# Kernel optimization log

Hardware: AMD Instinct MI355X
Metric: run time of the kernel (lower is better)

## Reference

```python
import jax, jax.numpy as jnp
import numpy as np

D_MODEL = 1024
NUM_HEADS = 16
D_K = D_MODEL // NUM_HEADS


def setup_inputs() -> dict:
    key = jax.random.key(0)
    ks = jax.random.split(key, 9)
    B, S = 2, 2048
    s = 1.0 / np.sqrt(D_MODEL)
    inp = {
        "x": jax.random.normal(ks[0], (B, S, D_MODEL), dtype=jnp.float32),
        "Wq": jax.random.normal(ks[1], (D_MODEL, D_MODEL), dtype=jnp.float32) * s,
        "bq": jnp.zeros((D_MODEL,), dtype=jnp.float32),
        "Wk": jax.random.normal(ks[2], (D_MODEL, D_MODEL), dtype=jnp.float32) * s,
        "bk": jnp.zeros((D_MODEL,), dtype=jnp.float32),
        "Wv": jax.random.normal(ks[3], (D_MODEL, D_MODEL), dtype=jnp.float32) * s,
        "bv": jnp.zeros((D_MODEL,), dtype=jnp.float32),
        "Wo": jax.random.normal(ks[4], (D_MODEL, D_MODEL), dtype=jnp.float32) * s,
        "bo": jnpp if False else jnp.zeros((D_MODEL,), dtype=jnp.float32),
    }
    return inp


def reference(x, Wq, bq, Wk, bk, Wv, bv, Wo, bo):
    B, S, _ = x.shape
    H, Dk = NUM_HEADS, D_K

    def proj(W, b):
        # [B,S,D] -> [B,H,S,Dk]
        return (x @ W + b).reshape(B, S, H, Dk).transpose(0, 2, 1, 3)

    Q = proj(Wq, bq)
    K = proj(Wk, bk)
    V = proj(Wv, bv)

    scores = jnp.einsum("bhqd,bhkd->bhqk", Q, K) / np.sqrt(Dk)
    attn = jax.nn.softmax(scores, axis=-1)  # no mask, dropout p=0 (eval)
    out = jnp.einsum("bhqk,bhkd->bhqd", attn, V)
    out = out.transpose(0, 2, 1, 3).reshape(B, S, D_MODEL)
    return out @ Wo + bo
```

## Files before the change

### kernel.cpp

```cpp
#include <hip/hip_runtime.h>
#include <hip/hip_bf16.h>
#include <cstdint>
#include <math.h>

#define D_MODEL 1024
#define NHEADS  16
#define DK      64
#define BATCH   2
#define SEQ     2048
#define M_TOTAL (BATCH*SEQ)
#define NSPLIT  2
#define NTS     (SEQ/64/NSPLIT)

using f32x4  = __attribute__((ext_vector_type(4)))  float;
using f32x16 = __attribute__((ext_vector_type(16))) float;
using s16x8  = __attribute__((ext_vector_type(8)))  short;

#define CSC (0.125f * 1.44269504088896341f)

__device__ __forceinline__ unsigned short bf16r(float f) {
    __hip_bfloat16 h = __float2bfloat16(f);
    return *(unsigned short*)&h;
}
__device__ __forceinline__ uint32_t cvtpk(float lo, float hi) {
    uint32_t r;
    asm("v_cvt_pk_bf16_f32 %0, %1, %2" : "=v"(r) : "v"(lo), "v"(hi));
    return r;
}
__device__ __forceinline__ float b2f(unsigned short u) {
    uint32_t x = (uint32_t)u << 16;
    float f;
    __builtin_memcpy(&f, &x, 4);
    return f;
}

__global__ __launch_bounds__(256) void conv_all(const float* __restrict__ x,
                                                unsigned short* __restrict__ xb,
                                                const float* __restrict__ W0, const float* __restrict__ W1,
                                                const float* __restrict__ W2, const float* __restrict__ W3,
                                                unsigned short* __restrict__ T0, unsigned short* __restrict__ T1,
                                                unsigned short* __restrict__ T2, unsigned short* __restrict__ T3)
{
    __shared__ float tile[32][33];
    const int bid = blockIdx.x;
    const int t   = threadIdx.x;

    if (bid < 2048) {
        const size_t i = ((size_t)bid * 256 + t) * 8;
        const float4 a = *(const float4*)(x + i);
        const float4 b = *(const float4*)(x + i + 4);
        ushort4 r0, r1;
        r0.x = bf16r(a.x); r0.y = bf16r(a.y); r0.z = bf16r(a.z); r0.w = bf16r(a.w);
        r1.x = bf16r(b.x); r1.y = bf16r(b.y); r1.z = bf16r(b.z); r1.w = bf16r(b.w);
        *(ushort4*)(xb + i)     = r0;
        *(ushort4*)(xb + i + 4) = r1;
        return;
    }

    const int b2   = bid - 2048;
    const int z    = b2 >> 10;
    const int rest = b2 & 1023;
    const int kblk = rest & 31;
    const int nblk = rest >> 5;
    const float* W; unsigned short* T;
    switch (z) {
        case 0: W = W0; T = T0; break;
        case 1: W = W1; T = T1; break;
        case 2: W = W2; T = T2; break;
        default: W = W3; T = T3; break;
    }
    const int r  = t >> 3;
    const int c4 = (t & 7) * 4;
    const int k0 = kblk * 32;
    const int n0 = nblk * 32;

    const float4 v = *(const float4*)(W + (size_t)(k0 + r) * 1024 + n0 + c4);
    tile[r][c4 + 0] = v.x; tile[r][c4 + 1] = v.y; tile[r][c4 + 2] = v.z; tile[r][c4 + 3] = v.w;
    __syncthreads();
    ushort4 o;
    o.x = bf16r(tile[c4 + 0][r]);
    o.y = bf16r(tile[c4 + 1][r]);
    o.z = bf16r(tile[c4 + 2][r]);
    o.w = bf16r(tile[c4 + 3][r]);
    *(ushort4*)(T + (size_t)(n0 + r) * 1024 + k0 + c4) = o;
}

template<int OUT_BF16>
__device__ __forceinline__ void gemm_mfma_body(const unsigned short* __restrict__ A,
                                               const unsigned short* __restrict__ Bt,
                                               const float* __restrict__ bias,
                                               void* __restrict__ C,
                                               float oscale, int m0, int n0)
{
    __shared__ unsigned short As[128 * 64];
    __shared__ unsigned short Bs[128 * 64];

    const int t    = threadIdx.x;
    const int w    = t >> 6;
    const int lane = t & 63;
    const int ln   = lane & 15;
    const int g    = lane >> 4;
    const int wr   = w >> 1, wc = w & 1;

    f32x4 acc[4][4];
#pragma unroll
    for (int mi = 0; mi < 4; ++mi)
#pragma unroll
        for (int ni = 0; ni < 4; ++ni)
#pragma unroll
            for (int j = 0; j < 4; ++j) acc[mi][ni][j] = 0.f;

    const int lrow = lane >> 3;
    const int lchk = (lane & 7) ^ lrow;
    const unsigned short* Ag = A  + (size_t)(m0 + w * 32 + lrow) * 1024 + lchk * 8;
    const unsigned short* Bg = Bt + (size_t)(n0 + w * 32 + lrow) * 1024 + lchk * 8;

    for (int kt = 0; kt < 16; ++kt) {
        const int k0 = kt * 64;
#pragma unroll
        for (int i = 0; i < 4; ++i) {
            __builtin_amdgcn_global_load_lds(Ag + (size_t)i * 8 * 1024 + k0,
                                             &As[(w * 32 + i * 8) * 64], 16, 0, 0);
            __builtin_amdgcn_global_load_lds(Bg + (size_t)i * 8 * 1024 + k0,
                                             &Bs[(w * 32 + i * 8) * 64], 16, 0, 0);
        }
        __syncthreads();

#pragma unroll
        for (int ks = 0; ks < 2; ++ks) {
            s16x8 af[4], bf[4];
#pragma unroll
            for (int mi = 0; mi < 4; ++mi) {
                const int row = wr * 64 + mi * 16 + ln;
                af[mi] = *(const s16x8*)((const char*)As + row * 128 +
                                         (((ks * 4 + g) ^ (ln & 7)) * 16));
            }
#pragma unroll
            for (int ni = 0; ni < 4; ++ni) {
                const int row = wc * 64 + ni * 16 + ln;
                bf[ni] = *(const s16x8*)((const char*)Bs + row * 128 +
                                         (((ks * 4 + g) ^ (ln & 7)) * 16));
            }
#pragma unroll
            for (int mi = 0; mi < 4; ++mi)
#pragma unroll
                for (int ni = 0; ni < 4; ++ni)
                    acc[mi][ni] = __builtin_amdgcn_mfma_f32_16x16x32_bf16(
                        af[mi], bf[ni], acc[mi][ni], 0, 0, 0);
        }
        __syncthreads();
    }

#pragma unroll
    for (int ni = 0; ni < 4; ++ni) {
        const int n = n0 + wc * 64 + ni * 16 + ln;
        const float bn = bias[n];
#pragma unroll
        for (int mi = 0; mi < 4; ++mi) {
            const int m = m0 + wr * 64 + mi * 16 + g * 4;
#pragma unroll
            for (int j = 0; j < 4; ++j) {
                const float v = (acc[mi][ni][j] + bn) * oscale;
                if constexpr (OUT_BF16)
                    ((unsigned short*)C)[(size_t)(m + j) * 1024 + n] = bf16r(v);
                else
                    ((float*)C)[(size_t)(m + j) * 1024 + n] = v;
            }
        }
    }
}

__global__ __launch_bounds__(256) void qkv_mfma(const unsigned short* __restrict__ xb,
                                                const unsigned short* __restrict__ Wqt, const float* __restrict__ bq,
                                                const unsigned short* __restrict__ Wkt, const float* __restrict__ bk,
                                                const unsigned short* __restrict__ Wvt, const float* __restrict__ bv,
                                                unsigned short* __restrict__ Q,
                                                unsigned short* __restrict__ K,
                                                unsigned short* __restrict__ V)
{
    const int bid = blockIdx.x;
    const int m   = bid / 24;
    const int rr  = bid - m * 24;
    const int z   = rr >> 3;
    const int n   = rr & 7;
    const int m0  = m * 128;
    const int n0  = n * 128;

    if (z == 0)      gemm_mfma_body<1>(xb, Wqt, bq, Q, CSC, m0, n0);
    else if (z == 1) gemm_mfma_body<1>(xb, Wkt, bk, K, 1.0f, m0, n0);
    else             gemm_mfma_body<1>(xb, Wvt, bv, V, 1.0f, m0, n0);
}

__global__ __launch_bounds__(256) void oproj_mfma(const unsigned short* __restrict__ Ab,
                                                  const unsigned short* __restrict__ Wot,
                                                  const float* __restrict__ bo,
                                                  float* __restrict__ C)
{
    gemm_mfma_body<0>(Ab, Wot, bo, C, 1.0f, blockIdx.y * 128, blockIdx.x * 128);
}

__global__ __launch_bounds__(256, 4) void attn_mfma(const unsigned short* __restrict__ Qb,
                                                    const unsigned short* __restrict__ Kb,
                                                    const unsigned short* __restrict__ Vb,
                                                    unsigned short* __restrict__ O0,
                                                    unsigned short* __restrict__ O1,
                                                    float* __restrict__ lbuf)
{
    __shared__ unsigned short Klds [64 * 64];
    __shared__ unsigned short Vtlds[64 * 64];

    const int t   = threadIdx.x;
    const int wid = t >> 6;
    const int l   = t & 63;
    const int q32 = l & 31;
    const int hi  = l >> 5;

    const int bid = blockIdx.x;
    const int grp = bid & 63;
    const int qb  = bid >> 6;
    const int bh  = grp >> 1;
    const int sp  = grp & 1;
    const int b   = bh >> 4;
    const int h   = bh & 15;
    const int qbase = qb * 128 + wid * 32;
    const size_t qrow = (size_t)(b * SEQ + qbase + q32);
    const size_t kv0  = (size_t)(b * SEQ) + (size_t)sp * (SEQ / NSPLIT);

    s16x8 qf[4];
    {
        const unsigned short* qp = Qb + qrow * D_MODEL + h * DK + 8 * hi;
#pragma unroll
        for (int ks = 0; ks < 4; ++ks) qf[ks] = *(const s16x8*)(qp + 16 * ks);
    }

    f32x16 ot0, ot1;
#pragma unroll
    for (int i = 0; i < 16; ++i) { ot0[i] = 0.f; ot1[i] = 0.f; }
    float lsum = 0.f;

    const int skey = t >> 3;
    const int sc8  = t & 7;
    const int vk2  = 2 * (t & 31);
    const int pk2  = (vk2 & ~12) | ((vk2 & 4) << 1) | ((vk2 & 8) >> 1);
    const int vd0  = 8 * (t >> 5);
    const unsigned short* Kg = Kb + (kv0 + skey) * D_MODEL + h * DK + 8 * sc8;
    const unsigned short* Vg = Vb + (kv0 + vk2) * D_MODEL + h * DK + vd0;
    char* const kw0 = (char*)Klds + skey * 128        + 16 * (sc8 ^ (skey & 7));
    char* const kw1 = (char*)Klds + (skey + 32) * 128 + 16 * (sc8 ^ (skey & 7));

    s16x8 kr0, kr1, vr0, vr1;

    auto load_regs = [&](int kt) {
        const size_t off = (size_t)kt * 64 * D_MODEL;
        kr0 = *(const s16x8*)(Kg + off);
        kr1 = *(const s16x8*)(Kg + off + (size_t)32 * D_MODEL);
        vr0 = *(const s16x8*)(Vg + off);
        vr1 = *(const s16x8*)(Vg + off + D_MODEL);
    };
    auto write_stage = [&]() {
        *(s16x8*)kw0 = kr0;
        *(s16x8*)kw1 = kr1;
#pragma unroll
        for (int i = 0; i < 8; ++i) {
            const int d = vd0 + i;
            const uint32_t val = (uint32_t)(unsigned short)vr0[i] |
                                 ((uint32_t)(unsigned short)vr1[i] << 16);
            *(uint32_t*)((char*)Vtlds + d * 128 +
                         16 * ((pk2 >> 3) ^ (d & 7)) + (pk2 & 7) * 2) = val;
        }
    };

    load_regs(0);
    write_stage();
    __syncthreads();

    for (int kt = 0; kt < NTS; ++kt) {
        if (kt < NTS - 1) load_regs(kt + 1);

        f32x16 s0, s1;
#pragma unroll
        for (int i = 0; i < 16; ++i) { s0[i] = 0.f; s1[i] = 0.f; }
        __builtin_amdgcn_s_setprio(1);
#pragma unroll
        for (int ks = 0; ks < 4; ++ks) {
            const int c = hi + 2 * ks;
            const s16x8 a0 = *(const s16x8*)((char*)Klds + q32 * 128 + 16 * (c ^ (q32 & 7)));
            const s16x8 a1 = *(const s16x8*)((char*)Klds + (q32 + 32) * 128 + 16 * (c ^ (q32 & 7)));
            s0 = __builtin_amdgcn_mfma_f32_32x32x16_bf16(a0, qf[ks], s0, 0, 0, 0);
            s1 = __builtin_amdgcn_mfma_f32_32x32x16_bf16(a1, qf[ks], s1, 0, 0, 0);
        }
        __builtin_amdgcn_s_setprio(0);

        float la = 0.f, lb = 0.f, lc = 0.f, ld = 0.f;
#pragma unroll
        for (int i = 0; i < 4; ++i) {
            s0[4 * i + 0] = exp2f(s0[4 * i + 0]); la += s0[4 * i + 0];
            s0[4 * i + 1] = exp2f(s0[4 * i + 1]); lb += s0[4 * i + 1];
            s0[4 * i + 2] = exp2f(s0[4 * i + 2]); lc += s0[4 * i + 2];
            s0[4 * i + 3] = exp2f(s0[4 * i + 3]); ld += s0[4 * i + 3];
            s1[4 * i + 0] = exp2f(s1[4 * i + 0]); la += s1[4 * i + 0];
            s1[4 * i + 1] = exp2f(s1[4 * i + 1]); lb += s1[4 * i + 1];
            s1[4 * i + 2] = exp2f(s1[4 * i + 2]); lc += s1[4 * i + 2];
            s1[4 * i + 3] = exp2f(s1[4 * i + 3]); ld += s1[4 * i + 3];
        }
        lsum += (la + lb) + (lc + ld);

        s16x8 pf[4];
        {
            union { uint32_t u[4]; s16x8 v; } F;
#pragma unroll
            for (int e = 0; e < 4; ++e) F.u[e] = cvtpk(s0[2 * e], s0[2 * e + 1]);
            pf[0] = F.v;
#pragma unroll
            for (int e = 0; e < 4; ++e) F.u[e] = cvtpk(s0[8 + 2 * e], s0[9 + 2 * e]);
            pf[1] = F.v;
#pragma unroll
            for (int e = 0; e < 4; ++e) F.u[e] = cvtpk(s1[2 * e], s1[2 * e + 1]);
            pf[2] = F.v;
#pragma unroll
            for (int e = 0; e < 4; ++e) F.u[e] = cvtpk(s1[8 + 2 * e], s1[9 + 2 * e]);
            pf[3] = F.v;
        }

        __builtin_amdgcn_s_setprio(1);
#pragma unroll
        for (int ks = 0; ks < 4; ++ks) {
            const int c = hi + 2 * ks;
            const s16x8 av0 = *(const s16x8*)((char*)Vtlds + q32 * 128 + 16 * (c ^ (q32 & 7)));
            const s16x8 av1 = *(const s16x8*)((char*)Vtlds + (q32 + 32) * 128 + 16 * (c ^ (q32 & 7)));
            ot0 = __builtin_amdgcn_mfma_f32_32x32x16_bf16(av0, pf[ks], ot0, 0, 0, 0);
            ot1 = __builtin_amdgcn_mfma_f32_32x32x16_bf16(av1, pf[ks], ot1, 0, 0, 0);
        }
        __builtin_amdgcn_s_setprio(0);

        __syncthreads();
        if (kt < NTS - 1) write_stage();
        __syncthreads();
    }

    const float ltot = lsum + __shfl_xor(lsum, 32);
    const size_t prow = (size_t)bh * SEQ + qbase + q32;
    if (hi == 0)
        lbuf[(size_t)sp * (BATCH * NHEADS * SEQ) + prow] = ltot;

    unsigned short* op = ((sp == 0) ? O0 : O1) + prow * DK;
#pragma unroll
    for (int j = 0; j < 4; ++j) {
        uint2 st0, st1;
        st0.x = cvtpk(ot0[4 * j + 0], ot0[4 * j + 1]);
        st0.y = cvtpk(ot0[4 * j + 2], ot0[4 * j + 3]);
        st1.x = cvtpk(ot1[4 * j + 0], ot1[4 * j + 1]);
        st1.y = cvtpk(ot1[4 * j + 2], ot1[4 * j + 3]);
        *(uint2*)(op + 8 * j + 4 * hi)      = st0;
        *(uint2*)(op + 32 + 8 * j + 4 * hi) = st1;
    }
}

__global__ __launch_bounds__(256) void attn_combine(const unsigned short* __restrict__ O0,
                                                    const unsigned short* __restrict__ O1,
                                                    const float* __restrict__ lbuf,
                                                    unsigned short* __restrict__ Ab)
{
    const int tid = blockIdx.x * 256 + threadIdx.x;
    const int row = tid >> 3;
    const int d0  = (tid & 7) * 8;
    const size_t NROW = (size_t)BATCH * NHEADS * SEQ;

    const float rinv = 1.0f / (lbuf[row] + lbuf[NROW + row]);

    const size_t src = (size_t)row * DK + d0;
    const ushort4 a0 = *(const ushort4*)(O0 + src);
    const ushort4 a1 = *(const ushort4*)(O0 + src + 4);
    const ushort4 b0 = *(const ushort4*)(O1 + src);
    const ushort4 b1 = *(const ushort4*)(O1 + src + 4);

    const int bh = row >> 11, s = row & 2047;
    const int b = bh >> 4, h = bh & 15;
    unsigned short* dst = Ab + ((size_t)(b * SEQ + s)) * D_MODEL + h * DK + d0;

    ushort4 o0, o1;
    o0.x = bf16r((b2f(a0.x) + b2f(b0.x)) * rinv);
    o0.y = bf16r((b2f(a0.y) + b2f(b0.y)) * rinv);
    o0.z = bf16r((b2f(a0.z) + b2f(b0.z)) * rinv);
    o0.w = bf16r((b2f(a0.w) + b2f(b0.w)) * rinv);
    o1.x = bf16r((b2f(a1.x) + b2f(b1.x)) * rinv);
    o1.y = bf16r((b2f(a1.y) + b2f(b1.y)) * rinv);
    o1.z = bf16r((b2f(a1.z) + b2f(b1.z)) * rinv);
    o1.w = bf16r((b2f(a1.w) + b2f(b1.w)) * rinv);
    *(ushort4*)(dst)     = o0;
    *(ushort4*)(dst + 4) = o1;
}

extern "C" void kernel_launch(void* const* d_in, const int* in_sizes, int n_in,
                              void* d_out, int out_size, void* d_ws, size_t ws_size,
                              hipStream_t stream)
{
    const float* x  = (const float*)d_in[0];
    const float* Wq = (const float*)d_in[1];
    const float* bq = (const float*)d_in[2];
    const float* Wk = (const float*)d_in[3];
    const float* bk = (const float*)d_in[4];
    const float* Wv = (const float*)d_in[5];
    const float* bv = (const float*)d_in[6];
    const float* Wo = (const float*)d_in[7];
    const float* bo = (const float*)d_in[8];

    float* out = (float*)d_out;

    const size_t mat  = (size_t)M_TOTAL * D_MODEL;
    const size_t wmat = (size_t)D_MODEL * D_MODEL;
    unsigned short* xb  = (unsigned short*)d_ws;
    unsigned short* Wqt = xb  + mat;
    unsigned short* Wkt = Wqt + wmat;
    unsigned short* Wvt = Wkt + wmat;
    unsigned short* Wot = Wvt + wmat;
    unsigned short* Qb  = Wot + wmat;
    unsigned short* Kb  = Qb  + mat;
    unsigned short* Vb  = Kb  + mat;
    unsigned short* Ab  = Vb  + mat;
    unsigned short* Op0 = Ab  + mat;
    unsigned short* Op1 = Op0 + mat;
    float*          lbuf = (float*)xb;

    conv_all<<<dim3(6144), 256, 0, stream>>>(x, xb, Wq, Wk, Wv, Wo, Wqt, Wkt, Wvt, Wot);

    qkv_mfma<<<dim3(32 * 24), 256, 0, stream>>>(xb, Wqt, bq, Wkt, bk, Wvt, bv, Qb, Kb, Vb);

    attn_mfma<<<dim3((SEQ / 128) * BATCH * NHEADS * NSPLIT), 256, 0, stream>>>(
        Qb, Kb, Vb, Op0, Op1, lbuf);

    attn_combine<<<dim3((BATCH * NHEADS * SEQ * 8) / 256), 256, 0, stream>>>(
        Op0, Op1, lbuf, Ab);

    oproj_mfma<<<dim3(8, 32), 256, 0, stream>>>(Ab, Wot, bo, out);
}
```

Baseline: 136.5 us.

## Double-buffer K/V LDS tiles and interleave two key tiles per attention iteration

Result: slower. 147.3 us (+7.9%).

```diff
diff --git a/kernel.cpp b/kernel.cpp
--- a/kernel.cpp
+++ b/kernel.cpp
@@ -199,15 +199,15 @@
     gemm_mfma_body<0>(Ab, Wot, bo, C, 1.0f, blockIdx.y * 128, blockIdx.x * 128);
 }
 
-__global__ __launch_bounds__(256, 4) void attn_mfma(const unsigned short* __restrict__ Qb,
+__global__ __launch_bounds__(256, 3) void attn_mfma(const unsigned short* __restrict__ Qb,
                                                     const unsigned short* __restrict__ Kb,
                                                     const unsigned short* __restrict__ Vb,
                                                     unsigned short* __restrict__ O0,
                                                     unsigned short* __restrict__ O1,
                                                     float* __restrict__ lbuf)
 {
-    __shared__ unsigned short Klds [64 * 64];
-    __shared__ unsigned short Vtlds[64 * 64];
+    __shared__ unsigned short Klds [2][64 * 64];
+    __shared__ unsigned short Vtlds[2][64 * 64];
 
     const int t   = threadIdx.x;
     const int wid = t >> 6;
@@ -245,8 +245,8 @@
     const int vd0  = 8 * (t >> 5);
     const unsigned short* Kg = Kb + (kv0 + skey) * D_MODEL + h * DK + 8 * sc8;
     const unsigned short* Vg = Vb + (kv0 + vk2) * D_MODEL + h * DK + vd0;
-    char* const kw0 = (char*)Klds + skey * 128        + 16 * (sc8 ^ (skey & 7));
-    char* const kw1 = (char*)Klds + (skey + 32) * 128 + 16 * (sc8 ^ (skey & 7));
+    const int kwo0 = skey * 128        + 16 * (sc8 ^ (skey & 7));
+    const int kwo1 = (skey + 32) * 128 + 16 * (sc8 ^ (skey & 7));
 
     s16x8 kr0, kr1, vr0, vr1;
 
@@ -257,85 +257,103 @@
         vr0 = *(const s16x8*)(Vg + off);
         vr1 = *(const s16x8*)(Vg + off + D_MODEL);
     };
-    auto write_stage = [&]() {
-        *(s16x8*)kw0 = kr0;
-        *(s16x8*)kw1 = kr1;
+    auto write_stage = [&](int buf) {
+        *(s16x8*)((char*)&Klds[buf][0] + kwo0) = kr0;
+        *(s16x8*)((char*)&Klds[buf][0] + kwo1) = kr1;
 #pragma unroll
         for (int i = 0; i < 8; ++i) {
             const int d = vd0 + i;
             const uint32_t val = (uint32_t)(unsigned short)vr0[i] |
                                  ((uint32_t)(unsigned short)vr1[i] << 16);
-            *(uint32_t*)((char*)Vtlds + d * 128 +
+            *(uint32_t*)((char*)&Vtlds[buf][0] + d * 128 +
                          16 * ((pk2 >> 3) ^ (d & 7)) + (pk2 & 7) * 2) = val;
         }
     };
 
-    load_regs(0);
-    write_stage();
-    __syncthreads();
-
-    for (int kt = 0; kt < NTS; ++kt) {
-        if (kt < NTS - 1) load_regs(kt + 1);
-
-        f32x16 s0, s1;
-#pragma unroll
-        for (int i = 0; i < 16; ++i) { s0[i] = 0.f; s1[i] = 0.f; }
+    auto qk = [&](int buf, f32x16& s0v, f32x16& s1v) {
+        const char* Kl = (const char*)&Klds[buf][0];
         __builtin_amdgcn_s_setprio(1);
 #pragma unroll
         for (int ks = 0; ks < 4; ++ks) {
             const int c = hi + 2 * ks;
-            const s16x8 a0 = *(const s16x8*)((char*)Klds + q32 * 128 + 16 * (c ^ (q32 & 7)));
-            const s16x8 a1 = *(const s16x8*)((char*)Klds + (q32 + 32) * 128 + 16 * (c ^ (q32 & 7)));
-            s0 = __builtin_amdgcn_mfma_f32_32x32x16_bf16(a0, qf[ks], s0, 0, 0, 0);
-            s1 = __builtin_amdgcn_mfma_f32_32x32x16_bf16(a1, qf[ks], s1, 0, 0, 0);
+            const s16x8 a0 = *(const s16x8*)(Kl + q32 * 128 + 16 * (c ^ (q32 & 7)));
+            const s16x8 a1 = *(const s16x8*)(Kl + (q32 + 32) * 128 + 16 * (c ^ (q32 & 7)));
+            s0v = __builtin_amdgcn_mfma_f32_32x32x16_bf16(a0, qf[ks], s0v, 0, 0, 0);
+            s1v = __builtin_amdgcn_mfma_f32_32x32x16_bf16(a1, qf[ks], s1v, 0, 0, 0);
         }
         __builtin_amdgcn_s_setprio(0);
-
+    };
+    auto smpack = [&](f32x16& s0v, f32x16& s1v, s16x8* pf) {
         float la = 0.f, lb = 0.f, lc = 0.f, ld = 0.f;
 #pragma unroll
         for (int i = 0; i < 4; ++i) {
-            s0[4 * i + 0] = exp2f(s0[4 * i + 0]); la += s0[4 * i + 0];
-            s0[4 * i + 1] = exp2f(s0[4 * i + 1]); lb += s0[4 * i + 1];
-            s0[4 * i + 2] = exp2f(s0[4 * i + 2]); lc += s0[4 * i + 2];
-            s0[4 * i + 3] = exp2f(s0[4 * i + 3]); ld += s0[4 * i + 3];
-            s1[4 * i + 0] = exp2f(s1[4 * i + 0]); la += s1[4 * i + 0];
-            s1[4 * i + 1] = exp2f(s1[4 * i + 1]); lb += s1[4 * i + 1];
-            s1[4 * i + 2] = exp2f(s1[4 * i + 2]); lc += s1[4 * i + 2];
-            s1[4 * i + 3] = exp2f(s1[4 * i + 3]); ld += s1[4 * i + 3];
+            s0v[4 * i + 0] = exp2f(s0v[4 * i + 0]); la += s0v[4 * i + 0];
+            s0v[4 * i + 1] = exp2f(s0v[4 * i + 1]); lb += s0v[4 * i + 1];
+            s0v[4 * i + 2] = exp2f(s0v[4 * i + 2]); lc += s0v[4 * i + 2];
+            s0v[4 * i + 3] = exp2f(s0v[4 * i + 3]); ld += s0v[4 * i + 3];
+            s1v[4 * i + 0] = exp2f(s1v[4 * i + 0]); la += s1v[4 * i + 0];
+            s1v[4 * i + 1] = exp2f(s1v[4 * i + 1]); lb += s1v[4 * i + 1];
+            s1v[4 * i + 2] = exp2f(s1v[4 * i + 2]); lc += s1v[4 * i + 2];
+            s1v[4 * i + 3] = exp2f(s1v[4 * i + 3]); ld += s1v[4 * i + 3];
         }
         lsum += (la + lb) + (lc + ld);
-
-        s16x8 pf[4];
-        {
-            union { uint32_t u[4]; s16x8 v; } F;
-#pragma unroll
-            for (int e = 0; e < 4; ++e) F.u[e] = cvtpk(s0[2 * e], s0[2 * e + 1]);
-            pf[0] = F.v;
-#pragma unroll
-            for (int e = 0; e < 4; ++e) F.u[e] = cvtpk(s0[8 + 2 * e], s0[9 + 2 * e]);
-            pf[1] = F.v;
-#pragma unroll
-            for (int e = 0; e < 4; ++e) F.u[e] = cvtpk(s1[2 * e], s1[2 * e + 1]);
-            pf[2] = F.v;
-#pragma unroll
-            for (int e = 0; e < 4; ++e) F.u[e] = cvtpk(s1[8 + 2 * e], s1[9 + 2 * e]);
-            pf[3] = F.v;
-        }
-
+        union { uint32_t u[4]; s16x8 v; } F;
+#pragma unroll
+        for (int e = 0; e < 4; ++e) F.u[e] = cvtpk(s0v[2 * e], s0v[2 * e + 1]);
+        pf[0] = F.v;
+#pragma unroll
+        for (int e = 0; e < 4; ++e) F.u[e] = cvtpk(s0v[8 + 2 * e], s0v[9 + 2 * e]);
+        pf[1] = F.v;
+#pragma unroll
+        for (int e = 0; e < 4; ++e) F.u[e] = cvtpk(s1v[2 * e], s1v[2 * e + 1]);
+        pf[2] = F.v;
+#pragma unroll
+        for (int e = 0; e < 4; ++e) F.u[e] = cvtpk(s1v[8 + 2 * e], s1v[9 + 2 * e]);
+        pf[3] = F.v;
+    };
+    auto pv = [&](int buf, const s16x8* pf) {
+        const char* Vl = (const char*)&Vtlds[buf][0];
         __builtin_amdgcn_s_setprio(1);
 #pragma unroll
         for (int ks = 0; ks < 4; ++ks) {
             const int c = hi + 2 * ks;
-            const s16x8 av0 = *(const s16x8*)((char*)Vtlds + q32 * 128 + 16 * (c ^ (q32 & 7)));
-            const s16x8 av1 = *(const s16x8*)((char*)Vtlds + (q32 + 32) * 128 + 16 * (c ^ (q32 & 7)));
+            const s16x8 av0 = *(const s16x8*)(Vl + q32 * 128 + 16 * (c ^ (q32 & 7)));
+            const s16x8 av1 = *(const s16x8*)(Vl + (q32 + 32) * 128 + 16 * (c ^ (q32 & 7)));
             ot0 = __builtin_amdgcn_mfma_f32_32x32x16_bf16(av0, pf[ks], ot0, 0, 0, 0);
             ot1 = __builtin_amdgcn_mfma_f32_32x32x16_bf16(av1, pf[ks], ot1, 0, 0, 0);
         }
         __builtin_amdgcn_s_setprio(0);
+    };
+
+    load_regs(0);
+    write_stage(0);
+    load_regs(1);
+    __syncthreads();
+    write_stage(1);
+    load_regs(2);
+    __syncthreads();
+
+    for (int i = 0; i < NTS / 2; ++i) {
+        f32x16 s0A, s1A, s0B, s1B;
+#pragma unroll
+        for (int k = 0; k < 16; ++k) { s0A[k] = 0.f; s1A[k] = 0.f; s0B[k] = 0.f; s1B[k] = 0.f; }
+
+        s16x8 pfA[4], pfB[4];
+        qk(0, s0A, s1A);
+        smpack(s0A, s1A, pfA);
+        qk(1, s0B, s1B);
+        pv(0, pfA);
+        smpack(s0B, s1B, pfB);
+        pv(1, pfB);
 
         __syncthreads();
-        if (kt < NTS - 1) write_stage();
-        __syncthreads();
+        if (i < NTS / 2 - 1) {
+            write_stage(0);
+            load_regs(2 * i + 3);
+            write_stage(1);
+            if (i < NTS / 2 - 2) load_regs(2 * i + 4);
+            __syncthreads();
+        }
     }
 
     const float ltot = lsum + __shfl_xor(lsum, 32);
```

## Fuse attention split-combine into output projection GEMM A-tile loading

Applied to the files above, without the earlier changes.

Measured after the change: 144.7 us. +6.0%, slower.

```diff
diff --git a/kernel.cpp b/kernel.cpp
--- a/kernel.cpp
+++ b/kernel.cpp
@@ -191,12 +191,103 @@
     else             gemm_mfma_body<1>(xb, Wvt, bv, V, 1.0f, m0, n0);
 }
 
-__global__ __launch_bounds__(256) void oproj_mfma(const unsigned short* __restrict__ Ab,
-                                                  const unsigned short* __restrict__ Wot,
-                                                  const float* __restrict__ bo,
-                                                  float* __restrict__ C)
-{
-    gemm_mfma_body<0>(Ab, Wot, bo, C, 1.0f, blockIdx.y * 128, blockIdx.x * 128);
+__global__ __launch_bounds__(256) void oproj_fused(const unsigned short* __restrict__ Op0,
+                                                   const unsigned short* __restrict__ Op1,
+                                                   const float* __restrict__ lbuf,
+                                                   const unsigned short* __restrict__ Wot,
+                                                   const float* __restrict__ bo,
+                                                   float* __restrict__ C)
+{
+    __shared__ unsigned short As[128 * 64];
+    __shared__ unsigned short Bs[128 * 64];
+
+    const int t    = threadIdx.x;
+    const int w    = t >> 6;
+    const int lane = t & 63;
+    const int ln   = lane & 15;
+    const int g    = lane >> 4;
+    const int wr   = w >> 1, wc = w & 1;
+    const int m0   = blockIdx.y * 128;
+    const int n0   = blockIdx.x * 128;
+    const size_t NROW = (size_t)BATCH * NHEADS * SEQ;
+
+    f32x4 acc[4][4];
+#pragma unroll
+    for (int mi = 0; mi < 4; ++mi)
+#pragma unroll
+        for (int ni = 0; ni < 4; ++ni)
+#pragma unroll
+            for (int j = 0; j < 4; ++j) acc[mi][ni][j] = 0.f;
+
+    const int lrow = lane >> 3;
+    const int lchk = (lane & 7) ^ lrow;
+    const int c8   = lane & 7;
+    const unsigned short* Bg = Wot + (size_t)(n0 + w * 32 + lrow) * 1024 + lchk * 8;
+
+    for (int kt = 0; kt < 16; ++kt) {
+        const int k0 = kt * 64;
+#pragma unroll
+        for (int i = 0; i < 4; ++i)
+            __builtin_amdgcn_global_load_lds(Bg + (size_t)i * 8 * 1024 + k0,
+                                             &Bs[(w * 32 + i * 8) * 64], 16, 0, 0);
+#pragma unroll
+        for (int i = 0; i < 4; ++i) {
+            const int row = w * 32 + i * 8 + lrow;
+            const int m   = m0 + row;
+            const int bb  = m >> 11;
+            const int s   = m & 2047;
+            const size_t prow = (size_t)(bb * 16 + kt) * 2048 + s;
+            const float rinv = 1.0f / (lbuf[prow] + lbuf[NROW + prow]);
+            const s16x8 u = *(const s16x8*)(Op0 + prow * DK + c8 * 8);
+            const s16x8 v = *(const s16x8*)(Op1 + prow * DK + c8 * 8);
+            union { uint32_t u32[4]; s16x8 v16; } F;
+#pragma unroll
+            for (int e = 0; e < 4; ++e) {
+                const float lo = (b2f((unsigned short)u[2 * e])     + b2f((unsigned short)v[2 * e]))     * rinv;
+                const float hi = (b2f((unsigned short)u[2 * e + 1]) + b2f((unsigned short)v[2 * e + 1])) * rinv;
+                F.u32[e] = cvtpk(lo, hi);
+            }
+            *(s16x8*)((char*)As + row * 128 + 16 * (c8 ^ lrow)) = F.v16;
+        }
+        __syncthreads();
+
+#pragma unroll
+        for (int ks = 0; ks < 2; ++ks) {
+            s16x8 af[4], bf[4];
+#pragma unroll
+            for (int mi = 0; mi < 4; ++mi) {
+                const int row = wr * 64 + mi * 16 + ln;
+                af[mi] = *(const s16x8*)((const char*)As + row * 128 +
+                                         (((ks * 4 + g) ^ (ln & 7)) * 16));
+            }
+#pragma unroll
+            for (int ni = 0; ni < 4; ++ni) {
+                const int row = wc * 64 + ni * 16 + ln;
+                bf[ni] = *(const s16x8*)((const char*)Bs + row * 128 +
+                                         (((ks * 4 + g) ^ (ln & 7)) * 16));
+            }
+#pragma unroll
+            for (int mi = 0; mi < 4; ++mi)
+#pragma unroll
+                for (int ni = 0; ni < 4; ++ni)
+                    acc[mi][ni] = __builtin_amdgcn_mfma_f32_16x16x32_bf16(
+                        af[mi], bf[ni], acc[mi][ni], 0, 0, 0);
+        }
+        __syncthreads();
+    }
+
+#pragma unroll
+    for (int ni = 0; ni < 4; ++ni) {
+        const int n = n0 + wc * 64 + ni * 16 + ln;
+        const float bn = bo[n];
+#pragma unroll
+        for (int mi = 0; mi < 4; ++mi) {
+            const int m = m0 + wr * 64 + mi * 16 + g * 4;
+#pragma unroll
+            for (int j = 0; j < 4; ++j)
+                C[(size_t)(m + j) * 1024 + n] = acc[mi][ni][j] + bn;
+        }
+    }
 }
 
 __global__ __launch_bounds__(256, 4) void attn_mfma(const unsigned short* __restrict__ Qb,
@@ -356,41 +447,6 @@
     }
 }
 
-__global__ __launch_bounds__(256) void attn_combine(const unsigned short* __restrict__ O0,
-                                                    const unsigned short* __restrict__ O1,
-                                                    const float* __restrict__ lbuf,
-                                                    unsigned short* __restrict__ Ab)
-{
-    const int tid = blockIdx.x * 256 + threadIdx.x;
-    const int row = tid >> 3;
-    const int d0  = (tid & 7) * 8;
-    const size_t NROW = (size_t)BATCH * NHEADS * SEQ;
-
-    const float rinv = 1.0f / (lbuf[row] + lbuf[NROW + row]);
-
-    const size_t src = (size_t)row * DK + d0;
-    const ushort4 a0 = *(const ushort4*)(O0 + src);
-    const ushort4 a1 = *(const ushort4*)(O0 + src + 4);
-    const ushort4 b0 = *(const ushort4*)(O1 + src);
-    const ushort4 b1 = *(const ushort4*)(O1 + src + 4);
-
-    const int bh = row >> 11, s = row & 2047;
-    const int b = bh >> 4, h = bh & 15;
-    unsigned short* dst = Ab + ((size_t)(b * SEQ + s)) * D_MODEL + h * DK + d0;
-
-    ushort4 o0, o1;
-    o0.x = bf16r((b2f(a0.x) + b2f(b0.x)) * rinv);
-    o0.y = bf16r((b2f(a0.y) + b2f(b0.y)) * rinv);
-    o0.z = bf16r((b2f(a0.z) + b2f(b0.z)) * rinv);
-    o0.w = bf16r((b2f(a0.w) + b2f(b0.w)) * rinv);
-    o1.x = bf16r((b2f(a1.x) + b2f(b1.x)) * rinv);
-    o1.y = bf16r((b2f(a1.y) + b2f(b1.y)) * rinv);
-    o1.z = bf16r((b2f(a1.z) + b2f(b1.z)) * rinv);
-    o1.w = bf16r((b2f(a1.w) + b2f(b1.w)) * rinv);
-    *(ushort4*)(dst)     = o0;
-    *(ushort4*)(dst + 4) = o1;
-}
-
 extern "C" void kernel_launch(void* const* d_in, const int* in_sizes, int n_in,
                               void* d_out, int out_size, void* d_ws, size_t ws_size,
                               hipStream_t stream)
@@ -417,8 +473,7 @@
     unsigned short* Qb  = Wot + wmat;
     unsigned short* Kb  = Qb  + mat;
     unsigned short* Vb  = Kb  + mat;
-    unsigned short* Ab  = Vb  + mat;
-    unsigned short* Op0 = Ab  + mat;
+    unsigned short* Op0 = Vb  + mat + mat;
     unsigned short* Op1 = Op0 + mat;
     float*          lbuf = (float*)xb;
 
@@ -429,8 +484,5 @@
     attn_mfma<<<dim3((SEQ / 128) * BATCH * NHEADS * NSPLIT), 256, 0, stream>>>(
         Qb, Kb, Vb, Op0, Op1, lbuf);
 
-    attn_combine<<<dim3((BATCH * NHEADS * SEQ * 8) / 256), 256, 0, stream>>>(
-        Op0, Op1, lbuf, Ab);
-
-    oproj_mfma<<<dim3(8, 32), 256, 0, stream>>>(Ab, Wot, bo, out);
-}
+    oproj_fused<<<dim3(8, 32), 256, 0, stream>>>(Op0, Op1, lbuf, Wot, bo, out);
+}
```
